# Kernel optimization log

Measured on AMD Instinct MI355X. Metric: run time of the kernel, lower is better.

Reference implementation:

```python
import jax, jax.numpy as jnp
import numpy as np

EMB, HEADS = 1024, 16
B, T = 4, 1024

def setup_inputs() -> dict:
    key = jax.random.key(0)
    ks = jax.random.split(key, 6)
    sc = 1.0 / np.sqrt(EMB)
    return {
        "x": jax.random.normal(ks[0], (B, T, EMB), jnp.float32),
        "Wq": jax.random.normal(ks[1], (EMB, EMB), jnp.float32) * sc,
        "Wk": jax.random.normal(ks[2], (EMB, EMB), jnp.float32) * sc,
        "Wv": jax.random.normal(ks[3], (EMB, EMB), jnp.float32) * sc,
        "Wo": jax.random.normal(ks[4], (EMB, EMB), jnp.float32) * sc,
        "bo": jnp.zeros((EMB,), jnp.float32),
    }

def reference(x, Wq, Wk, Wv, Wo, bo):
    b, t, e = x.shape
    h = HEADS
    s = e // h
    # nn.Linear(emb, emb, bias=False): y = x @ W.T
    q = (x @ Wq.T).reshape(b, t, h, s).transpose(0, 2, 1, 3)  # (b,h,t,s)
    k = (x @ Wk.T).reshape(b, t, h, s).transpose(0, 2, 1, 3)
    v = (x @ Wv.T).reshape(b, t, h, s).transpose(0, 2, 1, 3)
    scale = e ** 0.25  # original scales q and k each by emb**(1/4)
    q = q / scale
    k = k / scale
    dot = jnp.einsum('bhqs,bhks->bhqk', q, k)  # (b,h,t,t)
    # causal mask: strict upper triangle -> -inf (mask_diagonal=False)
    causal = jnp.tril(jnp.ones((t, t), dtype=bool))
    dot = jnp.where(causal[None, None], dot, -jnp.inf)
    attn = jax.nn.softmax(dot, axis=-1)
    out = jnp.einsum('bhqk,bhks->bhqs', attn, v)  # (b,h,t,s)
    out = out.transpose(0, 2, 1, 3).reshape(b, t, e)
    return out @ Wo.T + bo
```

## Files before the change

kernel.cpp:

```cpp
#include <hip/hip_runtime.h>
#include <hip/hip_bf16.h>
#include <stdint.h>


typedef __attribute__((ext_vector_type(8))) short short8;
typedef __attribute__((ext_vector_type(4))) float f32x4;
typedef __attribute__((ext_vector_type(16))) float f32x16;

__device__ __forceinline__ unsigned short f2bf(float f) {
    union { float f; unsigned int u; } v; v.f = f;
    unsigned int r = v.u + 0x7FFFu + ((v.u >> 16) & 1u);
    return (unsigned short)(r >> 16);
}

__device__ __forceinline__ void gload_lds16(const ushort* g, ushort* l) {
    __builtin_amdgcn_global_load_lds(
        (const __attribute__((address_space(1))) void*)g,
        (__attribute__((address_space(3))) void*)l,
        16, 0, 0);
}

__device__ __forceinline__ void wait_vmcnt_0() { asm volatile("s_waitcnt vmcnt(0)" ::: "memory"); }
__device__ __forceinline__ void wait_vmcnt_3() { asm volatile("s_waitcnt vmcnt(3)" ::: "memory"); }
__device__ __forceinline__ void wait_vmcnt_4() { asm volatile("s_waitcnt vmcnt(4)" ::: "memory"); }

__device__ __forceinline__ void block_barrier() {
    __builtin_amdgcn_sched_barrier(0);
    __builtin_amdgcn_s_barrier();
    __builtin_amdgcn_sched_barrier(0);
}

__global__ __launch_bounds__(256) void cast_bf16(
    const float* __restrict__ x,  const float* __restrict__ wq,
    const float* __restrict__ wk, const float* __restrict__ wv,
    const float* __restrict__ wo, ushort* __restrict__ dst)
{
    size_t e0 = (size_t)(blockIdx.x * 256 + threadIdx.x) * 4;
    const float* src; size_t off;
    if      (e0 < 4194304u) { src = x;  off = e0; }
    else if (e0 < 5242880u) { src = wq; off = e0 - 4194304u; }
    else if (e0 < 6291456u) { src = wk; off = e0 - 5242880u; }
    else if (e0 < 7340032u) { src = wv; off = e0 - 6291456u; }
    else                    { src = wo; off = e0 - 7340032u; }
    float4 v = *(const float4*)(src + off);
    ushort4 o;
    o.x = f2bf(v.x); o.y = f2bf(v.y); o.z = f2bf(v.z); o.w = f2bf(v.w);
    *(ushort4*)(dst + e0) = o;
}

template<int MODE, int BM, int WRg, int WCg>
__global__ __launch_bounds__(256) void gemm_bt(
    const ushort* __restrict__ A, const ushort* __restrict__ B,
    ushort* __restrict__ Qb, ushort* __restrict__ Kb, ushort* __restrict__ Vtb,
    float* __restrict__ Cout, const float* __restrict__ bias)
{
    constexpr int MF = BM / (32 * WRg);
    constexpr int NF = 128 / (32 * WCg);
    constexpr int NSTEP = 32;
    const int K = 1024;
    const int n0 = blockIdx.x * 128;
    const int m0 = blockIdx.y * BM;
    const int t  = threadIdx.x;
    const int w  = t >> 6, l = t & 63;
    const int l31 = l & 31, lh = l >> 5;
    const int wr = w / WCg, wc = w % WCg;

    __shared__ ushort As[3 * BM * 32];
    __shared__ ushort Bs[3 * 128 * 32];

    auto stage = [&](int j) {
        const int buf = j % 3;
        const int k0 = j * 32;
        #pragma unroll
        for (int i = 0; i < BM / 64; ++i) {
            int slot = i * 256 + t;
            int r = slot >> 2, blk = slot & 3;
            gload_lds16(A + (size_t)(m0 + r) * K + k0 + ((blk ^ ((r >> 1) & 3)) << 3),
                        &As[buf * BM * 32 + (i * 256 + w * 64) * 8]);
        }
        #pragma unroll
        for (int i = 0; i < 2; ++i) {
            int slot = i * 256 + t;
            int r = slot >> 2, blk = slot & 3;
            gload_lds16(B + (size_t)(n0 + r) * K + k0 + ((blk ^ ((r >> 1) & 3)) << 3),
                        &Bs[buf * 128 * 32 + (i * 256 + w * 64) * 8]);
        }
    };

    f32x16 acc[MF][NF] = {};

    stage(0); stage(1);
    for (int kt = 0; kt < NSTEP; ++kt) {
        if (kt < NSTEP - 1) { if (BM == 128) wait_vmcnt_4(); else wait_vmcnt_3(); }
        else wait_vmcnt_0();
        block_barrier();
        if (kt + 2 < NSTEP) stage(kt + 2);

        const ushort* Ab = &As[(kt % 3) * BM * 32];
        const ushort* Bb = &Bs[(kt % 3) * 128 * 32];
        #pragma unroll
        for (int kk = 0; kk < 2; ++kk) {
            const int c = kk * 2 + lh;
            short8 af[MF], bf[NF];
            #pragma unroll
            for (int mt = 0; mt < MF; ++mt) {
                int row = wr * (MF * 32) + mt * 32 + l31;
                af[mt] = *(const short8*)&Ab[row * 32 + ((c ^ ((row >> 1) & 3)) << 3)];
            }
            #pragma unroll
            for (int nt = 0; nt < NF; ++nt) {
                int row = wc * (NF * 32) + nt * 32 + l31;
                bf[nt] = *(const short8*)&Bb[row * 32 + ((c ^ ((row >> 1) & 3)) << 3)];
            }
            #pragma unroll
            for (int mt = 0; mt < MF; ++mt)
                #pragma unroll
                for (int nt = 0; nt < NF; ++nt)
                    acc[mt][nt] = __builtin_amdgcn_mfma_f32_32x32x16_bf16(
                        af[mt], bf[nt], acc[mt][nt], 0, 0, 0);
        }
    }

    if (MODE == 0) {
        #pragma unroll
        for (int mt = 0; mt < MF; ++mt) {
            int rbase = m0 + wr * (MF * 32) + mt * 32 + 4 * lh;
            #pragma unroll
            for (int nt = 0; nt < NF; ++nt) {
                int col = n0 + wc * (NF * 32) + nt * 32 + l31;
                int sel = col >> 10;
                int cw  = col & 1023;
                int h = cw >> 6, s = cw & 63;
                if (sel == 2) {
                    #pragma unroll
                    for (int rg = 0; rg < 4; ++rg) {
                        int tok = rbase + 8 * rg;
                        int b = tok >> 10, tq = tok & 1023;
                        ushort4 o;
                        o.x = f2bf(acc[mt][nt][rg * 4 + 0]);
                        o.y = f2bf(acc[mt][nt][rg * 4 + 1]);
                        o.z = f2bf(acc[mt][nt][rg * 4 + 2]);
                        o.w = f2bf(acc[mt][nt][rg * 4 + 3]);
                        *(ushort4*)&Vtb[(((size_t)(b * 16 + h)) * 64 + s) * 1024 + tq] = o;
                    }
                } else {
                    ushort* dst = (sel == 0) ? Qb : Kb;
                    float scl = (sel == 0) ? 0.03125f : 1.0f;
                    #pragma unroll
                    for (int reg = 0; reg < 16; ++reg) {
                        int tok = rbase + (reg & 3) + 8 * (reg >> 2);
                        int b = tok >> 10, tq = tok & 1023;
                        dst[(((size_t)(b * 16 + h)) * 1024 + tq) * 64 + s] =
                            f2bf(acc[mt][nt][reg] * scl);
                    }
                }
            }
        }
    } else {
        #pragma unroll
        for (int mt = 0; mt < MF; ++mt) {
            int rbase = m0 + wr * (MF * 32) + mt * 32 + 4 * lh;
            #pragma unroll
            for (int nt = 0; nt < NF; ++nt) {
                int col = n0 + wc * (NF * 32) + nt * 32 + l31;
                float bi = bias[col];
                #pragma unroll
                for (int reg = 0; reg < 16; ++reg) {
                    int row = rbase + (reg & 3) + 8 * (reg >> 2);
                    Cout[(size_t)row * 1024 + col] = acc[mt][nt][reg] + bi;
                }
            }
        }
    }
}

__global__ __launch_bounds__(256) void attn_kernel(
    const ushort* __restrict__ Q, const ushort* __restrict__ Kp,
    const ushort* __restrict__ Vt, ushort* __restrict__ O)
{
    const int id = blockIdx.x;
    const int half = id >> 8, jj = id & 255;
    const int qt = half ? 7 - (jj & 7) : (jj & 7);
    const int bh = (jj >> 3) + half * 32;
    const int t = threadIdx.x, w = t >> 6, l = t & 63;
    const int l15 = l & 15, l4 = l >> 4;

    __shared__ ushort Qs[128 * 64];
    __shared__ ushort Ks[3 * 64 * 64];
    __shared__ ushort Vts[3 * 64 * 64];
    __shared__ ushort Ps[4 * 32 * 64];

    const ushort* Qbase = Q  + ((size_t)bh * 1024 + (size_t)qt * 128) * 64;
    const ushort* Kbase = Kp + (size_t)bh * 1024 * 64;
    const ushort* Vtb   = Vt + (size_t)bh * 64 * 1024;

    auto stageKV = [&](int j) {
        const int buf = j % 3;
        #pragma unroll
        for (int i = 0; i < 2; ++i) {
            int slot = i * 256 + t; int r = slot >> 3, blk = slot & 7;
            gload_lds16(Kbase + (size_t)(j * 64 + r) * 64 + ((blk ^ (r & 7)) << 3),
                        &Ks[buf * 4096 + (i * 256 + w * 64) * 8]);
            gload_lds16(Vtb + (size_t)r * 1024 + j * 64 + ((blk ^ (r & 7)) << 3),
                        &Vts[buf * 4096 + (i * 256 + w * 64) * 8]);
        }
    };

    #pragma unroll
    for (int i = 0; i < 4; ++i) {
        int slot = i * 256 + t; int r = slot >> 3, blk = slot & 7;
        gload_lds16(Qbase + r * 64 + ((blk ^ (r & 7)) << 3), &Qs[(i * 256 + w * 64) * 8]);
    }
    const int nkv = 2 * qt + 2;
    stageKV(0);
    if (nkv > 1) stageKV(1);

    float l_acc[8];
    #pragma unroll
    for (int i = 0; i < 8; ++i) l_acc[i] = 0.f;
    f32x4 accO[2][4] = {};

    const int wqmin = qt * 128 + w * 32;
    for (int kvt = 0; kvt < nkv; ++kvt) {
        if (kvt < nkv - 1) wait_vmcnt_4(); else wait_vmcnt_0();
        block_barrier();
        if (kvt + 2 < nkv) stageKV(kvt + 2);

        const ushort* Kcur = &Ks[(kvt % 3) * 4096];
        const ushort* Vcur = &Vts[(kvt % 3) * 4096];

        if (kvt * 64 <= wqmin + 31) {
            f32x4 sf[2][4] = {};
            #pragma unroll
            for (int kk = 0; kk < 2; ++kk) {
                const int kblk = kk * 4 + l4;
                short8 qa[2], kb[4];
                #pragma unroll
                for (int mt = 0; mt < 2; ++mt) {
                    int row = w * 32 + mt * 16 + l15;
                    qa[mt] = *(const short8*)&Qs[row * 64 + ((kblk ^ (row & 7)) << 3)];
                }
                #pragma unroll
                for (int nt = 0; nt < 4; ++nt) {
                    int row = nt * 16 + l15;
                    kb[nt] = *(const short8*)&Kcur[row * 64 + ((kblk ^ (row & 7)) << 3)];
                }
                #pragma unroll
                for (int mt = 0; mt < 2; ++mt)
                    #pragma unroll
                    for (int nt = 0; nt < 4; ++nt)
                        sf[mt][nt] = __builtin_amdgcn_mfma_f32_16x16x32_bf16(
                            qa[mt], kb[nt], sf[mt][nt], 0, 0, 0);
            }

            const bool domask = (kvt * 64 + 63 > wqmin);
            #pragma unroll
            for (int mt = 0; mt < 2; ++mt) {
                #pragma unroll
                for (int r = 0; r < 4; ++r) {
                    const int qrow = wqmin + mt * 16 + l4 * 4 + r;
                    const int qlocal = mt * 16 + l4 * 4 + r;
                    const int idx = mt * 4 + r;
                    #pragma unroll
                    for (int nt = 0; nt < 4; ++nt) {
                        int col = kvt * 64 + nt * 16 + l15;
                        float p = (domask && col > qrow) ? 0.f : __expf(sf[mt][nt][r]);
                        l_acc[idx] += p;
                        int c = nt * 16 + l15;
                        Ps[w * 2048 + qlocal * 64 +
                           (((c >> 3) ^ (qlocal & 7)) << 3) + (c & 7)] = f2bf(p);
                    }
                }
            }
            asm volatile("s_waitcnt lgkmcnt(0)" ::: "memory");
            __builtin_amdgcn_sched_barrier(0);

            #pragma unroll
            for (int kk = 0; kk < 2; ++kk) {
                const int kblk = kk * 4 + l4;
                short8 pa[2], vb[4];
                #pragma unroll
                for (int mt = 0; mt < 2; ++mt) {
                    int row = mt * 16 + l15;
                    pa[mt] = *(const short8*)&Ps[w * 2048 + row * 64 + ((kblk ^ (row & 7)) << 3)];
                }
                #pragma unroll
                for (int st = 0; st < 4; ++st) {
                    int row = st * 16 + l15;
                    vb[st] = *(const short8*)&Vcur[row * 64 + ((kblk ^ (row & 7)) << 3)];
                }
                #pragma unroll
                for (int mt = 0; mt < 2; ++mt)
                    #pragma unroll
                    for (int st = 0; st < 4; ++st)
                        accO[mt][st] = __builtin_amdgcn_mfma_f32_16x16x32_bf16(
                            pa[mt], vb[st], accO[mt][st], 0, 0, 0);
            }
        }
    }

    const int b = bh >> 4, h = bh & 15;
    #pragma unroll
    for (int mt = 0; mt < 2; ++mt) {
        #pragma unroll
        for (int r = 0; r < 4; ++r) {
            float s = l_acc[mt * 4 + r];
            s += __shfl_xor(s, 1);
            s += __shfl_xor(s, 2);
            s += __shfl_xor(s, 4);
            s += __shfl_xor(s, 8);
            float inv = 1.0f / s;
            int tq = qt * 128 + w * 32 + mt * 16 + l4 * 4 + r;
            #pragma unroll
            for (int st = 0; st < 4; ++st) {
                int sc = st * 16 + l15;
                O[((size_t)b * 1024 + tq) * 1024 + h * 64 + sc] =
                    f2bf(accO[mt][st][r] * inv);
            }
        }
    }
}

extern "C" void kernel_launch(void* const* d_in, const int* in_sizes, int n_in,
                              void* d_out, int out_size, void* d_ws, size_t ws_size,
                              hipStream_t stream) {
    const float* x  = (const float*)d_in[0];
    const float* wq = (const float*)d_in[1];
    const float* wk = (const float*)d_in[2];
    const float* wv = (const float*)d_in[3];
    const float* wo = (const float*)d_in[4];
    const float* bo = (const float*)d_in[5];
    float* out = (float*)d_out;

    ushort* ws  = (ushort*)d_ws;
    ushort* xb  = ws;
    ushort* wb  = ws + (4u << 20);
    ushort* Qb  = ws + (8u << 20);
    ushort* Kb  = ws + (12u << 20);
    ushort* Vtb = ws + (16u << 20);
    ushort* Ob  = ws + (20u << 20);

    cast_bf16<<<8192, 256, 0, stream>>>(x, wq, wk, wv, wo, ws);
    gemm_bt<0, 128, 2, 2><<<dim3(24, 32), 256, 0, stream>>>(
        xb, wb, Qb, Kb, Vtb, nullptr, nullptr);
    attn_kernel<<<512, 256, 0, stream>>>(Qb, Kb, Vtb, Ob);
    gemm_bt<1, 64, 1, 4><<<dim3(8, 64), 256, 0, stream>>>(
        Ob, wb + (3u << 20), nullptr, nullptr, nullptr, out, bo);
}
```

Baseline: 104.8 us.

## Replace QKV projection GEMM with 256x256-tile 8-phase pipelined 512-thread kernel

Swaps the 128x128-tile QKV projection GEMM for a new kernel that uses 256x256 output tiles, 8 waves, 16x16x32 MFMAs and a double-buffered LDS schedule. Each K-step is split into eight phases that interleave global-to-LDS loads with LDS reads and MFMA bursts, and MFMA sections are raised in priority with s_setprio. A block-index swizzle is added for L2 locality. The aim is to reuse more data per tile and to hide load latency behind compute, at the cost of many more barriers, higher register and LDS use, and only 192 blocks, which may not fill every CU.

```diff
diff --git a/kernel.cpp b/kernel.cpp
--- a/kernel.cpp
+++ b/kernel.cpp
@@ -27,6 +27,10 @@
 __device__ __forceinline__ void block_barrier() {
     __builtin_amdgcn_sched_barrier(0);
     __builtin_amdgcn_s_barrier();
+    __builtin_amdgcn_sched_barrier(0);
+}
+__device__ __forceinline__ void lgk0() {
+    asm volatile("s_waitcnt lgkmcnt(0)" ::: "memory");
     __builtin_amdgcn_sched_barrier(0);
 }
 
@@ -48,6 +52,185 @@
     *(ushort4*)(dst + e0) = o;
 }
 
+__global__ __launch_bounds__(512) void gemm_qkv_8ph(
+    const ushort* __restrict__ A, const ushort* __restrict__ B,
+    ushort* __restrict__ Qb, ushort* __restrict__ Kb, ushort* __restrict__ Vtb)
+{
+    __shared__ ushort lds[2][2][2][128 * 64];
+
+    const int id = blockIdx.x;
+    const int swz = (id & 7) * 24 + (id >> 3);
+    const int bx = swz % 12, by = swz / 12;
+    const int n0 = bx * 256, m0 = by * 256;
+    const int t = threadIdx.x, w = t >> 6, l = t & 63;
+    const int l15 = l & 15, l4 = l >> 4;
+    const int wr = w >> 2, wc = w & 3;
+    const int K = 1024;
+
+    auto stage_half = [&](const ushort* gsrc, ushort* dst) {
+        #pragma unroll
+        for (int i = 0; i < 2; ++i) {
+            int slot = i * 512 + t;
+            int r = slot >> 3, blk = slot & 7;
+            gload_lds16(gsrc + (size_t)r * K + ((blk ^ (r & 7)) << 3),
+                        dst + (i * 512 + w * 64) * 8);
+        }
+    };
+    auto stageA = [&](int kt, int h, int buf) {
+        stage_half(A + (size_t)(m0 + h * 128) * K + kt * 64, &lds[buf][0][h][0]);
+    };
+    auto stageB = [&](int kt, int h, int buf) {
+        stage_half(B + (size_t)(n0 + h * 128) * K + kt * 64, &lds[buf][1][h][0]);
+    };
+
+    short8 af[8];
+    short8 vb0[4], vb1[4];
+    f32x4 acc[8][4] = {};
+
+    auto readA = [&](int buf, int qm) {
+        const ushort* base = &lds[buf][0][wr][0];
+        #pragma unroll
+        for (int kk = 0; kk < 2; ++kk)
+            #pragma unroll
+            for (int mt = 0; mt < 4; ++mt) {
+                int row = qm * 64 + mt * 16 + l15;
+                af[kk * 4 + mt] = *(const short8*)
+                    &base[row * 64 + (((kk * 4 + l4) ^ (row & 7)) << 3)];
+            }
+    };
+    auto readB0 = [&](int buf, int qn) {
+        const ushort* base = &lds[buf][1][wc >> 1][0];
+        #pragma unroll
+        for (int kk = 0; kk < 2; ++kk)
+            #pragma unroll
+            for (int nt = 0; nt < 2; ++nt) {
+                int row = (wc & 1) * 64 + qn * 32 + nt * 16 + l15;
+                vb0[kk * 2 + nt] = *(const short8*)
+                    &base[row * 64 + (((kk * 4 + l4) ^ (row & 7)) << 3)];
+            }
+    };
+    auto readB1 = [&](int buf, int qn) {
+        const ushort* base = &lds[buf][1][wc >> 1][0];
+        #pragma unroll
+        for (int kk = 0; kk < 2; ++kk)
+            #pragma unroll
+            for (int nt = 0; nt < 2; ++nt) {
+                int row = (wc & 1) * 64 + qn * 32 + nt * 16 + l15;
+                vb1[kk * 2 + nt] = *(const short8*)
+                    &base[row * 64 + (((kk * 4 + l4) ^ (row & 7)) << 3)];
+            }
+    };
+    auto mfma_vb0 = [&](int qm, int qn) {
+        __builtin_amdgcn_s_setprio(1);
+        #pragma unroll
+        for (int kk = 0; kk < 2; ++kk)
+            #pragma unroll
+            for (int mt = 0; mt < 4; ++mt)
+                #pragma unroll
+                for (int nt = 0; nt < 2; ++nt)
+                    acc[qm * 4 + mt][qn * 2 + nt] =
+                        __builtin_amdgcn_mfma_f32_16x16x32_bf16(
+                            af[kk * 4 + mt], vb0[kk * 2 + nt],
+                            acc[qm * 4 + mt][qn * 2 + nt], 0, 0, 0);
+        __builtin_amdgcn_s_setprio(0);
+    };
+    auto mfma_vb1 = [&](int qm, int qn) {
+        __builtin_amdgcn_s_setprio(1);
+        #pragma unroll
+        for (int kk = 0; kk < 2; ++kk)
+            #pragma unroll
+            for (int mt = 0; mt < 4; ++mt)
+                #pragma unroll
+                for (int nt = 0; nt < 2; ++nt)
+                    acc[qm * 4 + mt][qn * 2 + nt] =
+                        __builtin_amdgcn_mfma_f32_16x16x32_bf16(
+                            af[kk * 4 + mt], vb1[kk * 2 + nt],
+                            acc[qm * 4 + mt][qn * 2 + nt], 0, 0, 0);
+        __builtin_amdgcn_s_setprio(0);
+    };
+
+    stageB(0, 0, 0); stageB(0, 1, 0); stageA(0, 0, 0); stageA(0, 1, 0);
+    stageB(1, 0, 1); stageB(1, 1, 1);
+    wait_vmcnt_4();
+    block_barrier();
+
+    for (int j = 0; j < 8; ++j) {
+        const bool more = (j < 7);
+        readA(0, 0); readB0(0, 0);
+        stageA(2 * j + 1, 0, 1);
+        block_barrier(); lgk0();
+        mfma_vb0(0, 0);
+        block_barrier();
+        readB1(0, 1);
+        stageA(2 * j + 1, 1, 1);
+        block_barrier(); lgk0();
+        mfma_vb1(0, 1);
+        block_barrier();
+        readA(0, 1);
+        if (more) stageB(2 * j + 2, 0, 0);
+        block_barrier(); lgk0();
+        mfma_vb1(1, 1);
+        block_barrier();
+        if (more) stageB(2 * j + 2, 1, 0);
+        block_barrier(); lgk0();
+        mfma_vb0(1, 0);
+        if (more) wait_vmcnt_4(); else wait_vmcnt_0();
+        block_barrier();
+        readA(1, 0); readB0(1, 0);
+        if (more) stageA(2 * j + 2, 0, 0);
+        block_barrier(); lgk0();
+        mfma_vb0(0, 0);
+        block_barrier();
+        readB1(1, 1);
+        if (more) stageA(2 * j + 2, 1, 0);
+        block_barrier(); lgk0();
+        mfma_vb1(0, 1);
+        block_barrier();
+        readA(1, 1);
+        if (more) stageB(2 * j + 3, 0, 1);
+        block_barrier(); lgk0();
+        mfma_vb1(1, 1);
+        block_barrier();
+        if (more) stageB(2 * j + 3, 1, 1);
+        block_barrier(); lgk0();
+        mfma_vb0(1, 0);
+        if (more) { wait_vmcnt_4(); block_barrier(); }
+    }
+
+    #pragma unroll
+    for (int qm = 0; qm < 2; ++qm) {
+        #pragma unroll
+        for (int mt = 0; mt < 4; ++mt) {
+            int row = m0 + wr * 128 + qm * 64 + mt * 16 + l4 * 4;
+            int b = row >> 10, tq = row & 1023;
+            #pragma unroll
+            for (int qn = 0; qn < 2; ++qn) {
+                #pragma unroll
+                for (int nt = 0; nt < 2; ++nt) {
+                    int col = n0 + wc * 64 + qn * 32 + nt * 16 + l15;
+                    int sel = col >> 10;
+                    int cw  = col & 1023;
+                    int h = cw >> 6, s = cw & 63;
+                    f32x4 v = acc[qm * 4 + mt][qn * 2 + nt];
+                    if (sel == 2) {
+                        ushort4 o;
+                        o.x = f2bf(v[0]); o.y = f2bf(v[1]);
+                        o.z = f2bf(v[2]); o.w = f2bf(v[3]);
+                        *(ushort4*)&Vtb[(((size_t)(b * 16 + h)) * 64 + s) * 1024 + tq] = o;
+                    } else {
+                        ushort* dst = (sel == 0) ? Qb : Kb;
+                        float scl = (sel == 0) ? 0.03125f : 1.0f;
+                        #pragma unroll
+                        for (int jj = 0; jj < 4; ++jj)
+                            dst[(((size_t)(b * 16 + h)) * 1024 + tq + jj) * 64 + s] =
+                                f2bf(v[jj] * scl);
+                    }
+                }
+            }
+        }
+    }
+}
+
 template<int MODE, int BM, int WRg, int WCg>
 __global__ __launch_bounds__(256) void gemm_bt(
     const ushort* __restrict__ A, const ushort* __restrict__ B,
@@ -121,54 +304,17 @@
         }
     }
 
-    if (MODE == 0) {
-        #pragma unroll
-        for (int mt = 0; mt < MF; ++mt) {
-            int rbase = m0 + wr * (MF * 32) + mt * 32 + 4 * lh;
-            #pragma unroll
-            for (int nt = 0; nt < NF; ++nt) {
-                int col = n0 + wc * (NF * 32) + nt * 32 + l31;
-                int sel = col >> 10;
-                int cw  = col & 1023;
-                int h = cw >> 6, s = cw & 63;
-                if (sel == 2) {
-                    #pragma unroll
-                    for (int rg = 0; rg < 4; ++rg) {
-                        int tok = rbase + 8 * rg;
-                        int b = tok >> 10, tq = tok & 1023;
-                        ushort4 o;
-                        o.x = f2bf(acc[mt][nt][rg * 4 + 0]);
-                        o.y = f2bf(acc[mt][nt][rg * 4 + 1]);
-                        o.z = f2bf(acc[mt][nt][rg * 4 + 2]);
-                        o.w = f2bf(acc[mt][nt][rg * 4 + 3]);
-                        *(ushort4*)&Vtb[(((size_t)(b * 16 + h)) * 64 + s) * 1024 + tq] = o;
-                    }
-                } else {
-                    ushort* dst = (sel == 0) ? Qb : Kb;
-                    float scl = (sel == 0) ? 0.03125f : 1.0f;
-                    #pragma unroll
-                    for (int reg = 0; reg < 16; ++reg) {
-                        int tok = rbase + (reg & 3) + 8 * (reg >> 2);
-                        int b = tok >> 10, tq = tok & 1023;
-                        dst[(((size_t)(b * 16 + h)) * 1024 + tq) * 64 + s] =
-                            f2bf(acc[mt][nt][reg] * scl);
-                    }
-                }
-            }
-        }
-    } else {
-        #pragma unroll
-        for (int mt = 0; mt < MF; ++mt) {
-            int rbase = m0 + wr * (MF * 32) + mt * 32 + 4 * lh;
-            #pragma unroll
-            for (int nt = 0; nt < NF; ++nt) {
-                int col = n0 + wc * (NF * 32) + nt * 32 + l31;
-                float bi = bias[col];
-                #pragma unroll
-                for (int reg = 0; reg < 16; ++reg) {
-                    int row = rbase + (reg & 3) + 8 * (reg >> 2);
-                    Cout[(size_t)row * 1024 + col] = acc[mt][nt][reg] + bi;
-                }
+    #pragma unroll
+    for (int mt = 0; mt < MF; ++mt) {
+        int rbase = m0 + wr * (MF * 32) + mt * 32 + 4 * lh;
+        #pragma unroll
+        for (int nt = 0; nt < NF; ++nt) {
+            int col = n0 + wc * (NF * 32) + nt * 32 + l31;
+            float bi = bias[col];
+            #pragma unroll
+            for (int reg = 0; reg < 16; ++reg) {
+                int row = rbase + (reg & 3) + 8 * (reg >> 2);
+                Cout[(size_t)row * 1024 + col] = acc[mt][nt][reg] + bi;
             }
         }
     }
@@ -341,8 +487,7 @@
     ushort* Ob  = ws + (20u << 20);
 
     cast_bf16<<<8192, 256, 0, stream>>>(x, wq, wk, wv, wo, ws);
-    gemm_bt<0, 128, 2, 2><<<dim3(24, 32), 256, 0, stream>>>(
-        xb, wb, Qb, Kb, Vtb, nullptr, nullptr);
+    gemm_qkv_8ph<<<192, 512, 0, stream>>>(xb, wb, Qb, Kb, Vtb);
     attn_kernel<<<512, 256, 0, stream>>>(Qb, Kb, Vtb, Ob);
     gemm_bt<1, 64, 1, 4><<<dim3(8, 64), 256, 0, stream>>>(
         Ob, wb + (3u << 20), nullptr, nullptr, nullptr, out, bo);
```

New measurement: 102.7 us. 2.0% less time.
